# Kernel tuning notes

Measured on AMD Instinct MI355X. Metric: run time of the kernel, lower is better.

The kernel has to match this reference:

```python
import jax, jax.numpy as jnp
import numpy as np

K = (3, 5, 7)
TAU_MIN, TAU_MAX = 0.03, 0.5


def _l2norm(x, axis=1, eps=1e-12):
    # matches torch F.normalize: x / max(||x||, eps)
    n = jnp.sqrt(jnp.sum(x * x, axis=axis, keepdims=True))
    return x / jnp.maximum(n, eps)


def _affinity_one(feat, kappa_ch, qw_k, kw_k, k):
    # feat: (B, C, H, W); kappa_ch: (B, 1, H, W); qw_k/kw_k: (Ca, C)
    B, C, H, W = feat.shape
    q = jnp.einsum('bchw,oc->bohw', feat, qw_k)
    key = jnp.einsum('bchw,oc->bohw', feat, kw_k)
    qn = _l2norm(q)
    kn = _l2norm(key)
    p = k // 2
    knp = jnp.pad(kn, ((0, 0), (0, 0), (p, p), (p, p)))
    # windowed cosine correlation: loop over the small fixed set of k*k offsets
    sims = []
    for dy in range(k):
        for dx in range(k):
            sims.append(jnp.sum(qn * knp[:, :, dy:dy + H, dx:dx + W], axis=1))
    sim = jnp.stack(sims, axis=1)  # (B, k*k, H, W)
    # temperature from curvature: GLOBAL min/max over the sliced channel
    kmin = kappa_ch.min()
    kmax = kappa_ch.max()
    kap_n = (kappa_ch - kmin) / (kmax - kmin + 1e-06)
    tau = jnp.clip(TAU_MAX - kap_n * (TAU_MAX - TAU_MIN), TAU_MIN, TAU_MAX)
    return sim / (tau + 1e-06)  # broadcast (B,kk,H,W) / (B,1,H,W)


def setup_inputs() -> dict:
    key = jax.random.key(0)
    k1, k2, k3, k4 = jax.random.split(key, 4)
    B, C, H, W = 4, 64, 256, 256
    CA = 32
    feat = jax.random.normal(k1, (B, C, H, W), dtype=jnp.float32)
    kappa = jax.random.uniform(k2, (B, len(K), H, W), dtype=jnp.float32)
    scale = 1.0 / np.sqrt(C)
    qw = jax.random.normal(k3, (len(K), CA, C), dtype=jnp.float32) * scale
    kw = jax.random.normal(k4, (len(K), CA, C), dtype=jnp.float32) * scale
    return {'feat': feat, 'kappa': kappa, 'qw': qw, 'kw': kw}


def reference(feat, kappa, qw, kw):
    out = []
    for i, k in enumerate(K):
        out.append(_affinity_one(feat, kappa[:, i:i + 1], qw[i], kw[i], k))
    return tuple(out)
```

## Files before the change

kernel.cpp:

```cpp
#include <hip/hip_runtime.h>
#include <stdint.h>

#define HW   65536
#define IMG  256
#define NB   4
#define NC   64
#define NA   32

typedef __attribute__((ext_vector_type(8))) short short8v;
typedef __attribute__((ext_vector_type(4))) float f32x4;

__device__ __forceinline__ unsigned short f2bf(float x) {
  unsigned u = __float_as_uint(x);
  u += 0x7FFFu + ((u >> 16) & 1u);
  return (unsigned short)(u >> 16);
}
__device__ __forceinline__ float bfval(unsigned short h) { return __uint_as_float((unsigned)h << 16); }
__device__ __forceinline__ unsigned packbf(float a, float b) {
  return (unsigned)f2bf(a) | ((unsigned)f2bf(b) << 16);
}

__global__ void prep_afrag(const float* __restrict__ qw, const float* __restrict__ kw,
                           unsigned short* __restrict__ afrag, unsigned* __restrict__ mm) {
  int idx = blockIdx.x * 256 + threadIdx.x;
  if (blockIdx.x == 0 && threadIdx.x < 6)
    mm[threadIdx.x] = (threadIdx.x < 3) ? 0xFFFFFFFFu : 0u;
  if (idx >= 3 * 4 * 2 * 2 * 64 * 8) return;
  int j    = idx & 7;
  int lane = (idx >> 3) & 63;
  int h    = (idx >> 9) & 1;
  int ks   = (idx >> 10) & 1;
  int mt   = (idx >> 11) & 3;
  int i    = idx >> 13;
  int s = mt >> 1;
  int o = (mt & 1) * 16 + (lane & 15);
  int c = ks * 32 + (lane >> 4) * 8 + j;
  float v = (s ? kw : qw)[((size_t)i * NA + o) * NC + c];
  unsigned short hi = f2bf(v);
  afrag[idx] = h ? f2bf(v - bfval(hi)) : hi;
}

__global__ __launch_bounds__(256) void minmax_k(const float* __restrict__ kappa,
                                                unsigned* __restrict__ mm) {
  const int i = blockIdx.y;
  const unsigned* ku = (const unsigned*)kappa;
  unsigned lo = 0xFFFFFFFFu, hi = 0u;
  for (int idx = blockIdx.x * 256 + threadIdx.x; idx < NB * HW; idx += gridDim.x * 256) {
    int b = idx >> 16, p = idx & (HW - 1);
    unsigned v = ku[((size_t)(b * 3 + i)) * HW + p];
    lo = min(lo, v); hi = max(hi, v);
  }
#pragma unroll
  for (int d = 32; d >= 1; d >>= 1) {
    lo = min(lo, (unsigned)__shfl_xor((int)lo, d, 64));
    hi = max(hi, (unsigned)__shfl_xor((int)hi, d, 64));
  }
  __shared__ unsigned slo[4], shi[4];
  if ((threadIdx.x & 63) == 0) { slo[threadIdx.x >> 6] = lo; shi[threadIdx.x >> 6] = hi; }
  __syncthreads();
  if (threadIdx.x == 0) {
    lo = min(min(slo[0], slo[1]), min(slo[2], slo[3]));
    hi = max(max(shi[0], shi[1]), max(shi[2], shi[3]));
    atomicMin(&mm[i], lo);
    atomicMax(&mm[i + 3], hi);
  }
}

__global__ __launch_bounds__(256) void proj_all(const float* __restrict__ feat,
                                                const unsigned short* __restrict__ afr,
                                                unsigned* __restrict__ qb,
                                                unsigned* __restrict__ kb,
                                                const int nsl, const int i0) {
  const int t = blockIdx.x;
  const int b = t >> 8;
  const int p0 = (t & 255) * 256;
  const int lane = threadIdx.x & 63;
  const int w = threadIdx.x >> 6;
  const int pbase = p0 + w * 64;

  short8v bh[4][2], bl[4][2];
  const float* fb = feat + (size_t)b * NC * HW;
#pragma unroll
  for (int ks = 0; ks < 2; ++ks) {
    float fv[32];
#pragma unroll
    for (int nt = 0; nt < 4; ++nt) {
      const int px = pbase + nt * 16 + (lane & 15);
      const float* fp = fb + (size_t)(ks * 32 + (lane >> 4) * 8) * HW + px;
#pragma unroll
      for (int j = 0; j < 8; ++j) fv[nt * 8 + j] = fp[(size_t)j * HW];
    }
#pragma unroll
    for (int nt = 0; nt < 4; ++nt)
#pragma unroll
      for (int j = 0; j < 8; ++j) {
        float f = fv[nt * 8 + j];
        unsigned short h = f2bf(f);
        bh[nt][ks][j] = (short)h;
        bl[nt][ks][j] = (short)f2bf(f - bfval(h));
      }
  }

#pragma unroll 1
  for (int sl = 0; sl < nsl; ++sl) {
#pragma unroll 1
    for (int s = 0; s < 2; ++s) {
      const unsigned short* af = afr + (size_t)(i0 + sl) * 8192;

      short8v ah[2][2];
#pragma unroll
      for (int m = 0; m < 2; ++m)
#pragma unroll
        for (int ks = 0; ks < 2; ++ks) {
          int mt = s * 2 + m;
          ah[m][ks] = *(const short8v*)(af + (size_t)((mt * 2 + ks) * 2) * 512 + lane * 8);
        }

      f32x4 acc[2][4];
#pragma unroll
      for (int m = 0; m < 2; ++m)
#pragma unroll
        for (int nt = 0; nt < 4; ++nt) acc[m][nt] = (f32x4){0.f, 0.f, 0.f, 0.f};

#pragma unroll
      for (int nt = 0; nt < 4; ++nt)
#pragma unroll
        for (int ks = 0; ks < 2; ++ks)
#pragma unroll
          for (int m = 0; m < 2; ++m) {
            acc[m][nt] = __builtin_amdgcn_mfma_f32_16x16x32_bf16(ah[m][ks], bh[nt][ks], acc[m][nt], 0, 0, 0);
            acc[m][nt] = __builtin_amdgcn_mfma_f32_16x16x32_bf16(ah[m][ks], bl[nt][ks], acc[m][nt], 0, 0, 0);
          }

      unsigned* dstbuf = (s ? kb : qb) + (size_t)sl * NB * HW * 16;
#pragma unroll
      for (int nt = 0; nt < 4; ++nt) {
        float ssq = 0.f;
#pragma unroll
        for (int m = 0; m < 2; ++m)
#pragma unroll
          for (int r = 0; r < 4; ++r) ssq = fmaf(acc[m][nt][r], acc[m][nt][r], ssq);
        ssq += __shfl_xor(ssq, 16, 64);
        ssq += __shfl_xor(ssq, 32, 64);
        float inv = 1.0f / fmaxf(sqrtf(ssq), 1e-12f);
        const int px = pbase + nt * 16 + (lane & 15);
        const size_t pix = (size_t)b * HW + px;
#pragma unroll
        for (int m = 0; m < 2; ++m) {
          int c0 = m * 16 + (lane >> 4) * 4;
          uint2 v;
          v.x = packbf(acc[m][nt][0] * inv, acc[m][nt][1] * inv);
          v.y = packbf(acc[m][nt][2] * inv, acc[m][nt][3] * inv);
          *(uint2*)(dstbuf + pix * 16 + (c0 >> 1)) = v;
        }
      }
    }
  }
}

template <int KS>
__device__ __forceinline__ void corr_mfma_body(float* Csh,
                                               const unsigned* __restrict__ qn,
                                               const unsigned* __restrict__ kn,
                                               const float* __restrict__ kappa,
                                               const unsigned* __restrict__ mm,
                                               const int i, const int b,
                                               float* __restrict__ out) {
  constexpr int P = KS / 2;
  constexpr int KK = KS * KS;
  constexpr int CST = 20;
  constexpr int NCOL = 22;
  constexpr int YST = NCOL * CST;
  constexpr int NR = KS + 3;
  const int y0 = blockIdx.y * 16, x0 = blockIdx.x * 16;
  const int lane = threadIdx.x & 63, w = threadIdx.x >> 6;
  const int cq = lane & 15;
  const int rq = lane >> 4;
  const int y = y0 + w * 4 + rq;
  const int x = x0 + cq;
  float* Cw = Csh + w * (4 * YST);

  const int kx0 = x0 - P + cq;
  const int kx1 = kx0 + 16;
  const int kyb = y0 + w * 4 - P;
  const unsigned* knb = kn + (size_t)b * HW * 16;

  short8v B0r[NR], B1r[NR];
#pragma unroll
  for (int r = 0; r < NR; ++r) {
    short8v z = {0, 0, 0, 0, 0, 0, 0, 0};
    B0r[r] = z; B1r[r] = z;
    const int ky = kyb + r;
    if ((unsigned)ky < (unsigned)IMG) {
      const unsigned* krow = knb + (size_t)ky * IMG * 16;
      if ((unsigned)kx0 < (unsigned)IMG) B0r[r] = *(const short8v*)(krow + (size_t)kx0 * 16 + rq * 4);
      if ((unsigned)kx1 < (unsigned)IMG) B1r[r] = *(const short8v*)(krow + (size_t)kx1 * 16 + rq * 4);
    }
  }

  short8v A[4];
#pragma unroll
  for (int yl = 0; yl < 4; ++yl) {
    const unsigned* p = qn + ((size_t)b * HW + (size_t)(y0 + w * 4 + yl) * IMG + x0 + cq) * 16 + rq * 4;
    A[yl] = *(const short8v*)p;
  }

  float kap = kappa[((size_t)(b * 3 + i)) * HW + (size_t)y * IMG + x];
  float kmin = __uint_as_float(mm[i]);
  float kmax = __uint_as_float(mm[i + 3]);
  float kapn = (kap - kmin) / (kmax - kmin + 1e-6f);
  float tau = fminf(fmaxf(0.5f - kapn * (0.5f - 0.03f), 0.03f), 0.5f);
  float scale = 1.0f / (tau + 1e-6f);

#pragma unroll
  for (int dy = 0; dy < KS; ++dy) {
    asm volatile("" ::: "memory");
#pragma unroll
    for (int yl = 0; yl < 4; ++yl) {
      f32x4 a0 = {0.f, 0.f, 0.f, 0.f}, a1 = {0.f, 0.f, 0.f, 0.f};
      a0 = __builtin_amdgcn_mfma_f32_16x16x32_bf16(A[yl], B0r[yl + dy], a0, 0, 0, 0);
      a1 = __builtin_amdgcn_mfma_f32_16x16x32_bf16(A[yl], B1r[yl + dy], a1, 0, 0, 0);
      *(f32x4*)(Cw + yl * YST + cq * CST + rq * 4) = a0;
      if (cq < NCOL - 16)
        *(f32x4*)(Cw + yl * YST + (16 + cq) * CST + rq * 4) = a1;
    }
    asm volatile("s_waitcnt lgkmcnt(0)" ::: "memory");
    __builtin_amdgcn_sched_barrier(0);
    float* ob = out + ((size_t)b * KK + (size_t)dy * KS) * HW + (size_t)y * IMG + x;
#pragma unroll
    for (int dx = 0; dx < KS; ++dx) {
      float v = Cw[rq * YST + (cq + dx) * CST + cq];
      __builtin_nontemporal_store(v * scale, ob + (size_t)dx * HW);
    }
  }
}

__global__ __launch_bounds__(256) void corr_all(const unsigned* __restrict__ qb,
                                                const unsigned* __restrict__ kb,
                                                const float* __restrict__ kappa,
                                                const unsigned* __restrict__ mm,
                                                const int i0, float* __restrict__ out) {
  __shared__ __align__(16) float Csh[7040];
  const int g = blockIdx.z >> 2;
  const int b = blockIdx.z & 3;
  const int fused = (gridDim.z > 4) ? 1 : 0;
  const int i = fused ? (2 - g) : i0;
  const int slot = fused ? i : 0;
  const unsigned* qn = qb + (size_t)slot * NB * HW * 16;
  const unsigned* kn = kb + (size_t)slot * NB * HW * 16;
  const size_t plane = (size_t)NB * HW;
  if (i == 0)
    corr_mfma_body<3>(Csh, qn, kn, kappa, mm, 0, b, out);
  else if (i == 1)
    corr_mfma_body<5>(Csh, qn, kn, kappa, mm, 1, b, out + plane * 9);
  else
    corr_mfma_body<7>(Csh, qn, kn, kappa, mm, 2, b, out + plane * 34);
}

extern "C" void kernel_launch(void* const* d_in, const int* in_sizes, int n_in,
                              void* d_out, int out_size, void* d_ws, size_t ws_size,
                              hipStream_t stream) {
  const float* feat  = (const float*)d_in[0];
  const float* kappa = (const float*)d_in[1];
  const float* qw    = (const float*)d_in[2];
  const float* kw    = (const float*)d_in[3];
  float* out = (float*)d_out;

  char* ws = (char*)d_ws;
  unsigned* mm = (unsigned*)ws;
  unsigned short* afrag = (unsigned short*)(ws + 64);
  unsigned* qbuf = (unsigned*)(ws + 65536);

  const size_t slot = (size_t)NB * HW * 16;
  const size_t need3 = 65536 + (size_t)6 * slot * 4;
  const int fused = (ws_size >= need3) ? 1 : 0;
  const int nsl = fused ? 3 : 1;
  unsigned* kbuf = qbuf + (size_t)nsl * slot;

  hipLaunchKernelGGL(prep_afrag, dim3(96), dim3(256), 0, stream, qw, kw, afrag, mm);
  hipLaunchKernelGGL(minmax_k, dim3(64, 3), dim3(256), 0, stream, kappa, mm);

  if (fused) {
    hipLaunchKernelGGL(proj_all, dim3(NB * HW / 256), dim3(256), 0, stream,
                       feat, afrag, qbuf, kbuf, 3, 0);
    hipLaunchKernelGGL(corr_all, dim3(IMG / 16, IMG / 16, NB * 3), dim3(256), 0, stream,
                       qbuf, kbuf, kappa, mm, 0, out);
  } else {
    for (int i = 0; i < 3; ++i) {
      hipLaunchKernelGGL(proj_all, dim3(NB * HW / 256), dim3(256), 0, stream,
                         feat, afrag, qbuf, kbuf, 1, i);
      hipLaunchKernelGGL(corr_all, dim3(IMG / 16, IMG / 16, NB), dim3(256), 0, stream,
                         qbuf, kbuf, kappa, mm, i, out);
    }
  }
}
```

Before: 101.0 us.

## Fuse projection and windowed correlation into one kernel with LDS-staged q/k tiles

```diff
diff --git a/kernel.cpp b/kernel.cpp
--- a/kernel.cpp
+++ b/kernel.cpp
@@ -66,145 +66,158 @@
   }
 }
 
-__global__ __launch_bounds__(256) void proj_all(const float* __restrict__ feat,
-                                                const unsigned short* __restrict__ afr,
-                                                unsigned* __restrict__ qb,
-                                                unsigned* __restrict__ kb,
-                                                const int nsl, const int i0) {
-  const int t = blockIdx.x;
-  const int b = t >> 8;
-  const int p0 = (t & 255) * 256;
-  const int lane = threadIdx.x & 63;
-  const int w = threadIdx.x >> 6;
-  const int pbase = p0 + w * 64;
-
-  short8v bh[4][2], bl[4][2];
-  const float* fb = feat + (size_t)b * NC * HW;
-#pragma unroll
-  for (int ks = 0; ks < 2; ++ks) {
-    float fv[32];
-#pragma unroll
-    for (int nt = 0; nt < 4; ++nt) {
-      const int px = pbase + nt * 16 + (lane & 15);
-      const float* fp = fb + (size_t)(ks * 32 + (lane >> 4) * 8) * HW + px;
-#pragma unroll
-      for (int j = 0; j < 8; ++j) fv[nt * 8 + j] = fp[(size_t)j * HW];
-    }
-#pragma unroll
-    for (int nt = 0; nt < 4; ++nt)
-#pragma unroll
-      for (int j = 0; j < 8; ++j) {
-        float f = fv[nt * 8 + j];
-        unsigned short h = f2bf(f);
-        bh[nt][ks][j] = (short)h;
-        bl[nt][ks][j] = (short)f2bf(f - bfval(h));
-      }
-  }
+template <int KS>
+__device__ __forceinline__ void fused_body(unsigned* Lds,
+                                           const float* __restrict__ fb,
+                                           const unsigned short* __restrict__ af,
+                                           const float* __restrict__ kappa,
+                                           const unsigned* __restrict__ mm,
+                                           const int i, const int b,
+                                           float* __restrict__ out) {
+  constexpr int P = KS / 2;
+  constexpr int KK = KS * KS;
+  constexpr int NRB = 16 + 2 * P;
+  constexpr int NR = KS + 3;
+  constexpr int RPX = 24;
+  constexpr int CST = 20, NCOL = 22, YST = NCOL * CST;
+  const int y0 = blockIdx.y * 16, x0 = blockIdx.x * 16;
+  const int lane = threadIdx.x & 63, w = threadIdx.x >> 6;
+  const int cq = lane & 15, rq = lane >> 4;
+  unsigned* Kn = Lds;
+  unsigned* Qd = Lds + 23 * RPX * 16;
+
+  {
+    short8v Wk[2][2];
+#pragma unroll
+    for (int m = 0; m < 2; ++m)
+#pragma unroll
+      for (int ks = 0; ks < 2; ++ks)
+        Wk[m][ks] = *(const short8v*)(af + (size_t)((((2 + m) * 2 + ks) * 2)) * 512 + lane * 8);
 
 #pragma unroll 1
-  for (int sl = 0; sl < nsl; ++sl) {
-#pragma unroll 1
-    for (int s = 0; s < 2; ++s) {
-      const unsigned short* af = afr + (size_t)(i0 + sl) * 8192;
-
-      short8v ah[2][2];
-#pragma unroll
-      for (int m = 0; m < 2; ++m)
+    for (int r = w; r < NRB; r += 4) {
+      const int ky = y0 - P + r;
+      const bool rowok = (unsigned)ky < (unsigned)IMG;
+      const int kyc = rowok ? ky : 0;
+#pragma unroll
+      for (int ct = 0; ct < 2; ++ct) {
+        const int kx = x0 - P + ct * 16 + cq;
+        const bool ok = rowok && ((unsigned)kx < (unsigned)IMG);
+        const int kxc = ok ? kx : 0;
+        short8v bhv[2], blv[2];
 #pragma unroll
         for (int ks = 0; ks < 2; ++ks) {
-          int mt = s * 2 + m;
-          ah[m][ks] = *(const short8v*)(af + (size_t)((mt * 2 + ks) * 2) * 512 + lane * 8);
-        }
-
-      f32x4 acc[2][4];
-#pragma unroll
-      for (int m = 0; m < 2; ++m)
-#pragma unroll
-        for (int nt = 0; nt < 4; ++nt) acc[m][nt] = (f32x4){0.f, 0.f, 0.f, 0.f};
-
-#pragma unroll
-      for (int nt = 0; nt < 4; ++nt)
+          const float* fp = fb + (size_t)(ks * 32 + rq * 8) * HW + (size_t)kyc * IMG + kxc;
+          float fv[8];
+#pragma unroll
+          for (int j = 0; j < 8; ++j) fv[j] = fp[(size_t)j * HW];
+#pragma unroll
+          for (int j = 0; j < 8; ++j) {
+            float f = ok ? fv[j] : 0.f;
+            unsigned short h = f2bf(f);
+            bhv[ks][j] = (short)h;
+            blv[ks][j] = (short)f2bf(f - bfval(h));
+          }
+        }
+        f32x4 acc[2];
+        acc[0] = (f32x4){0.f, 0.f, 0.f, 0.f};
+        acc[1] = (f32x4){0.f, 0.f, 0.f, 0.f};
 #pragma unroll
         for (int ks = 0; ks < 2; ++ks)
 #pragma unroll
           for (int m = 0; m < 2; ++m) {
-            acc[m][nt] = __builtin_amdgcn_mfma_f32_16x16x32_bf16(ah[m][ks], bh[nt][ks], acc[m][nt], 0, 0, 0);
-            acc[m][nt] = __builtin_amdgcn_mfma_f32_16x16x32_bf16(ah[m][ks], bl[nt][ks], acc[m][nt], 0, 0, 0);
+            acc[m] = __builtin_amdgcn_mfma_f32_16x16x32_bf16(Wk[m][ks], bhv[ks], acc[m], 0, 0, 0);
+            acc[m] = __builtin_amdgcn_mfma_f32_16x16x32_bf16(Wk[m][ks], blv[ks], acc[m], 0, 0, 0);
           }
-
-      unsigned* dstbuf = (s ? kb : qb) + (size_t)sl * NB * HW * 16;
-#pragma unroll
-      for (int nt = 0; nt < 4; ++nt) {
         float ssq = 0.f;
 #pragma unroll
         for (int m = 0; m < 2; ++m)
 #pragma unroll
-          for (int r = 0; r < 4; ++r) ssq = fmaf(acc[m][nt][r], acc[m][nt][r], ssq);
+          for (int rr = 0; rr < 4; ++rr) ssq = fmaf(acc[m][rr], acc[m][rr], ssq);
         ssq += __shfl_xor(ssq, 16, 64);
         ssq += __shfl_xor(ssq, 32, 64);
         float inv = 1.0f / fmaxf(sqrtf(ssq), 1e-12f);
-        const int px = pbase + nt * 16 + (lane & 15);
-        const size_t pix = (size_t)b * HW + px;
+        if (ct == 0 || cq < RPX - 16) {
+          unsigned* rec = Kn + (((r * RPX) + ct * 16 + cq) << 4);
+#pragma unroll
+          for (int m = 0; m < 2; ++m) {
+            uint2 v;
+            v.x = packbf(acc[m][0] * inv, acc[m][1] * inv);
+            v.y = packbf(acc[m][2] * inv, acc[m][3] * inv);
+            *(uint2*)(rec + m * 8 + rq * 2) = v;
+          }
+        }
+      }
+    }
+  }
+
+  {
+    short8v Wq[2][2];
+#pragma unroll
+    for (int m = 0; m < 2; ++m)
+#pragma unroll
+      for (int ks = 0; ks < 2; ++ks)
+        Wq[m][ks] = *(const short8v*)(af + (size_t)(((m * 2 + ks) * 2)) * 512 + lane * 8);
+#pragma unroll
+    for (int yl = 0; yl < 4; ++yl) {
+      const int qy = y0 + w * 4 + yl;
+      short8v bhv[2], blv[2];
+#pragma unroll
+      for (int ks = 0; ks < 2; ++ks) {
+        const float* fp = fb + (size_t)(ks * 32 + rq * 8) * HW + (size_t)qy * IMG + x0 + cq;
+        float fv[8];
+#pragma unroll
+        for (int j = 0; j < 8; ++j) fv[j] = fp[(size_t)j * HW];
+#pragma unroll
+        for (int j = 0; j < 8; ++j) {
+          unsigned short h = f2bf(fv[j]);
+          bhv[ks][j] = (short)h;
+          blv[ks][j] = (short)f2bf(fv[j] - bfval(h));
+        }
+      }
+      f32x4 acc[2];
+      acc[0] = (f32x4){0.f, 0.f, 0.f, 0.f};
+      acc[1] = (f32x4){0.f, 0.f, 0.f, 0.f};
+#pragma unroll
+      for (int ks = 0; ks < 2; ++ks)
 #pragma unroll
         for (int m = 0; m < 2; ++m) {
-          int c0 = m * 16 + (lane >> 4) * 4;
-          uint2 v;
-          v.x = packbf(acc[m][nt][0] * inv, acc[m][nt][1] * inv);
-          v.y = packbf(acc[m][nt][2] * inv, acc[m][nt][3] * inv);
-          *(uint2*)(dstbuf + pix * 16 + (c0 >> 1)) = v;
-        }
+          acc[m] = __builtin_amdgcn_mfma_f32_16x16x32_bf16(Wq[m][ks], bhv[ks], acc[m], 0, 0, 0);
+          acc[m] = __builtin_amdgcn_mfma_f32_16x16x32_bf16(Wq[m][ks], blv[ks], acc[m], 0, 0, 0);
+        }
+      float ssq = 0.f;
+#pragma unroll
+      for (int m = 0; m < 2; ++m)
+#pragma unroll
+        for (int rr = 0; rr < 4; ++rr) ssq = fmaf(acc[m][rr], acc[m][rr], ssq);
+      ssq += __shfl_xor(ssq, 16, 64);
+      ssq += __shfl_xor(ssq, 32, 64);
+      float inv = 1.0f / fmaxf(sqrtf(ssq), 1e-12f);
+      unsigned* rec = Qd + ((((w * 4 + yl) * 16) + cq) << 4);
+#pragma unroll
+      for (int m = 0; m < 2; ++m) {
+        uint2 v;
+        v.x = packbf(acc[m][0] * inv, acc[m][1] * inv);
+        v.y = packbf(acc[m][2] * inv, acc[m][3] * inv);
+        *(uint2*)(rec + m * 8 + rq * 2) = v;
       }
     }
   }
-}
-
-template <int KS>
-__device__ __forceinline__ void corr_mfma_body(float* Csh,
-                                               const unsigned* __restrict__ qn,
-                                               const unsigned* __restrict__ kn,
-                                               const float* __restrict__ kappa,
-                                               const unsigned* __restrict__ mm,
-                                               const int i, const int b,
-                                               float* __restrict__ out) {
-  constexpr int P = KS / 2;
-  constexpr int KK = KS * KS;
-  constexpr int CST = 20;
-  constexpr int NCOL = 22;
-  constexpr int YST = NCOL * CST;
-  constexpr int NR = KS + 3;
-  const int y0 = blockIdx.y * 16, x0 = blockIdx.x * 16;
-  const int lane = threadIdx.x & 63, w = threadIdx.x >> 6;
-  const int cq = lane & 15;
-  const int rq = lane >> 4;
-  const int y = y0 + w * 4 + rq;
-  const int x = x0 + cq;
-  float* Cw = Csh + w * (4 * YST);
-
-  const int kx0 = x0 - P + cq;
-  const int kx1 = kx0 + 16;
-  const int kyb = y0 + w * 4 - P;
-  const unsigned* knb = kn + (size_t)b * HW * 16;
-
-  short8v B0r[NR], B1r[NR];
-#pragma unroll
-  for (int r = 0; r < NR; ++r) {
-    short8v z = {0, 0, 0, 0, 0, 0, 0, 0};
-    B0r[r] = z; B1r[r] = z;
-    const int ky = kyb + r;
-    if ((unsigned)ky < (unsigned)IMG) {
-      const unsigned* krow = knb + (size_t)ky * IMG * 16;
-      if ((unsigned)kx0 < (unsigned)IMG) B0r[r] = *(const short8v*)(krow + (size_t)kx0 * 16 + rq * 4);
-      if ((unsigned)kx1 < (unsigned)IMG) B1r[r] = *(const short8v*)(krow + (size_t)kx1 * 16 + rq * 4);
-    }
-  }
-
-  short8v A[4];
-#pragma unroll
-  for (int yl = 0; yl < 4; ++yl) {
-    const unsigned* p = qn + ((size_t)b * HW + (size_t)(y0 + w * 4 + yl) * IMG + x0 + cq) * 16 + rq * 4;
-    A[yl] = *(const short8v*)p;
-  }
-
+
+  __syncthreads();
+
+  short8v B0r[NR], B1r[NR], A[4];
+#pragma unroll
+  for (int t = 0; t < NR; ++t) {
+    const unsigned* base = Kn + ((((w * 4 + t) * RPX) + cq) << 4) + rq * 4;
+    B0r[t] = *(const short8v*)base;
+    B1r[t] = *(const short8v*)(base + 256);
+  }
+#pragma unroll
+  for (int yl = 0; yl < 4; ++yl)
+    A[yl] = *(const short8v*)(Qd + ((((w * 4 + yl) * 16) + cq) << 4) + rq * 4);
+
+  const int y = y0 + w * 4 + rq, x = x0 + cq;
   float kap = kappa[((size_t)(b * 3 + i)) * HW + (size_t)y * IMG + x];
   float kmin = __uint_as_float(mm[i]);
   float kmax = __uint_as_float(mm[i + 3]);
@@ -212,6 +225,9 @@
   float tau = fminf(fmaxf(0.5f - kapn * (0.5f - 0.03f), 0.03f), 0.5f);
   float scale = 1.0f / (tau + 1e-6f);
 
+  __syncthreads();
+
+  float* Cw = (float*)Lds + w * (4 * YST);
 #pragma unroll
   for (int dy = 0; dy < KS; ++dy) {
     asm volatile("" ::: "memory");
@@ -235,26 +251,24 @@
   }
 }
 
-__global__ __launch_bounds__(256) void corr_all(const unsigned* __restrict__ qb,
-                                                const unsigned* __restrict__ kb,
-                                                const float* __restrict__ kappa,
-                                                const unsigned* __restrict__ mm,
-                                                const int i0, float* __restrict__ out) {
-  __shared__ __align__(16) float Csh[7040];
+__global__ __launch_bounds__(256) void affin_all(const float* __restrict__ feat,
+                                                 const unsigned short* __restrict__ afr,
+                                                 const float* __restrict__ kappa,
+                                                 const unsigned* __restrict__ mm,
+                                                 float* __restrict__ out) {
+  __shared__ __align__(16) unsigned Lds[23 * 24 * 16 + 256 * 16];
   const int g = blockIdx.z >> 2;
   const int b = blockIdx.z & 3;
-  const int fused = (gridDim.z > 4) ? 1 : 0;
-  const int i = fused ? (2 - g) : i0;
-  const int slot = fused ? i : 0;
-  const unsigned* qn = qb + (size_t)slot * NB * HW * 16;
-  const unsigned* kn = kb + (size_t)slot * NB * HW * 16;
+  const int i = 2 - g;
+  const float* fb = feat + (size_t)b * NC * HW;
+  const unsigned short* af = afr + (size_t)i * 8192;
   const size_t plane = (size_t)NB * HW;
-  if (i == 0)
-    corr_mfma_body<3>(Csh, qn, kn, kappa, mm, 0, b, out);
+  if (i == 2)
+    fused_body<7>(Lds, fb, af, kappa, mm, 2, b, out + plane * 34);
   else if (i == 1)
-    corr_mfma_body<5>(Csh, qn, kn, kappa, mm, 1, b, out + plane * 9);
+    fused_body<5>(Lds, fb, af, kappa, mm, 1, b, out + plane * 9);
   else
-    corr_mfma_body<7>(Csh, qn, kn, kappa, mm, 2, b, out + plane * 34);
+    fused_body<3>(Lds, fb, af, kappa, mm, 0, b, out);
 }
 
 extern "C" void kernel_launch(void* const* d_in, const int* in_sizes, int n_in,
@@ -269,28 +283,9 @@
   char* ws = (char*)d_ws;
   unsigned* mm = (unsigned*)ws;
   unsigned short* afrag = (unsigned short*)(ws + 64);
-  unsigned* qbuf = (unsigned*)(ws + 65536);
-
-  const size_t slot = (size_t)NB * HW * 16;
-  const size_t need3 = 65536 + (size_t)6 * slot * 4;
-  const int fused = (ws_size >= need3) ? 1 : 0;
-  const int nsl = fused ? 3 : 1;
-  unsigned* kbuf = qbuf + (size_t)nsl * slot;
 
   hipLaunchKernelGGL(prep_afrag, dim3(96), dim3(256), 0, stream, qw, kw, afrag, mm);
   hipLaunchKernelGGL(minmax_k, dim3(64, 3), dim3(256), 0, stream, kappa, mm);
-
-  if (fused) {
-    hipLaunchKernelGGL(proj_all, dim3(NB * HW / 256), dim3(256), 0, stream,
-                       feat, afrag, qbuf, kbuf, 3, 0);
-    hipLaunchKernelGGL(corr_all, dim3(IMG / 16, IMG / 16, NB * 3), dim3(256), 0, stream,
-                       qbuf, kbuf, kappa, mm, 0, out);
-  } else {
-    for (int i = 0; i < 3; ++i) {
-      hipLaunchKernelGGL(proj_all, dim3(NB * HW / 256), dim3(256), 0, stream,
-                         feat, afrag, qbuf, kbuf, 1, i);
-      hipLaunchKernelGGL(corr_all, dim3(IMG / 16, IMG / 16, NB), dim3(256), 0, stream,
-                         qbuf, kbuf, kappa, mm, i, out);
-    }
-  }
-}
+  hipLaunchKernelGGL(affin_all, dim3(IMG / 16, IMG / 16, NB * 3), dim3(256), 0, stream,
+                     feat, afrag, kappa, mm, out);
+}
```

New measurement: 237.3 us. 135% more time.
